# Kernel optimization log

Hardware: AMD Instinct MI355X
Metric: run time of the kernel (lower is better)

Reference implementation:

```python
import jax, jax.numpy as jnp
import numpy as np

DIM = 768
HEADS = 12
FF = 3072
EPS = 1e-6


def setup_inputs() -> dict:
    key = jax.random.key(0)
    ks = jax.random.split(key, 12)
    B, S, D, F_ = 64, 197, DIM, FF
    s = 0.02
    inp = {
        "x": jax.random.normal(ks[0], (B, S, D), jnp.float32),
        "Wq": jax.random.normal(ks[1], (D, D), jnp.float32) * s,
        "bq": jnp.zeros((D,), jnp.float32),
        "Wk": jax.random.normal(ks[2], (D, D), jnp.float32) * s,
        "bk": jnp.zeros((D,), jnp.float32),
        "Wv": jax.random.normal(ks[3], (D, D), jnp.float32) * s,
        "bv": jnp.zeros((D,), jnp.float32),
        "Wo": jax.random.normal(ks[4], (D, D), jnp.float32) * s,
        "bo": jnp.zeros((D,), jnp.float32),
        "ln1_w": jnp.ones((D,), jnp.float32),
        "ln1_b": jnp.zeros((D,), jnp.float32),
        "W1": jax.random.normal(ks[5], (D, F_), jnp.float32) * s,
        "b1": jnp.zeros((F_,), jnp.float32),
        "W2": jax.random.normal(ks[6], (F_, D), jnp.float32) * s,
        "b2": jnp.zeros((D,), jnp.float32),
        "ln2_w": jnp.ones((D,), jnp.float32),
        "ln2_b": jnp.zeros((D,), jnp.float32),
        "mask": jnp.ones((B, S), jnp.int32),
    }
    return inp


def _layernorm(x, w, b):
    m = jnp.mean(x, axis=-1, keepdims=True)
    v = jnp.mean(jnp.square(x - m), axis=-1, keepdims=True)  # unbiased=False
    return (x - m) / jnp.sqrt(v + EPS) * w + b


def _block(x, mask_f, Wq, bq, Wk, bk, Wv, bv, Wo, bo, ln1_w, ln1_b, W1, b1, W2, b2, ln2_w, ln2_b):
    B, S, D = x.shape
    H = HEADS
    Dh = D // H
    # --- attention (pre-norm) ---
    h = _layernorm(x, ln1_w, ln1_b)
    q = (h @ Wq + bq).reshape(B, S, H, Dh).transpose(0, 2, 1, 3)
    k = (h @ Wk + bk).reshape(B, S, H, Dh).transpose(0, 2, 1, 3)
    v = (h @ Wv + bv).reshape(B, S, H, Dh).transpose(0, 2, 1, 3)
    scores = jnp.einsum("bhqd,bhkd->bhqk", q, k) / jnp.sqrt(jnp.float32(Dh))
    scores = scores - 10000.0 * (1.0 - mask_f[:, None, None, :])
    probs = jax.nn.softmax(scores, axis=-1)
    attn = jnp.einsum("bhqk,bhkd->bhqd", probs, v).transpose(0, 2, 1, 3).reshape(B, S, D)
    x = x + (attn @ Wo + bo)  # dropout = identity (eval)
    # --- FFN (pre-norm), exact erf GELU (F.gelu default) ---
    h = _layernorm(x, ln2_w, ln2_b)
    h = jax.nn.gelu(h @ W1 + b1, approximate=False)
    x = x + (h @ W2 + b2)
    return x


def reference(x, Wq, bq, Wk, bk, Wv, bv, Wo, bo, ln1_w, ln1_b, W1, b1, W2, b2, ln2_w, ln2_b, mask):
    mask_f = mask.astype(jnp.float32)
    return _block(x, mask_f, Wq, bq, Wk, bk, Wv, bv, Wo, bo, ln1_w, ln1_b, W1, b1, W2, b2, ln2_w, ln2_b)
```

## Files before the change

kernel.cpp:

```cpp
#include <hip/hip_runtime.h>
#include <stdint.h>

#define B_   64
#define S_   197
#define D_   768
#define H_   12
#define F_   3072
#define BS_  (B_ * S_)

typedef __attribute__((ext_vector_type(8))) short short8;
typedef __attribute__((ext_vector_type(4))) float f32x4;

__device__ __forceinline__ float bf2f(unsigned short h) {
    union { unsigned int u; float f; } v; v.u = ((unsigned int)h) << 16; return v.f;
}
__device__ __forceinline__ unsigned short f2bf(float f) {
    union { float f; unsigned int u; } v; v.f = f;
    unsigned int r = v.u + 0x7FFFu + ((v.u >> 16) & 1u);
    return (unsigned short)(r >> 16);
}

__device__ __forceinline__ void g2l16(const void* g, void* l) {
    __builtin_amdgcn_global_load_lds(
        (const __attribute__((address_space(1))) unsigned int*)g,
        (__attribute__((address_space(3))) unsigned int*)l, 16, 0, 0);
}

__device__ __forceinline__ float gelu_f(float c) {
    float z = fabsf(c) * 0.70710678118f;
    float t = __builtin_amdgcn_rcpf(1.f + 0.3275911f * z);
    float p = ((((1.061405429f * t - 1.453152027f) * t + 1.421413741f) * t
               - 0.284496736f) * t + 0.254829592f) * t;
    float erfv = 1.f - p * __expf(-z * z);
    erfv = c < 0.f ? -erfv : erfv;
    return 0.5f * c * (1.f + erfv);
}

__global__ __launch_bounds__(256)
void transpose_all(const float* __restrict__ Wq, const float* __restrict__ Wk,
                   const float* __restrict__ Wv, const float* __restrict__ Wo,
                   const float* __restrict__ W1, const float* __restrict__ W2,
                   const float* __restrict__ bq, const float* __restrict__ bk,
                   const float* __restrict__ bv,
                   unsigned short* __restrict__ wqkvT, unsigned short* __restrict__ woT,
                   unsigned short* __restrict__ w1T, unsigned short* __restrict__ w2T,
                   float* __restrict__ bcat) {
    int blk = blockIdx.x;
    int tx = threadIdx.x, ty = threadIdx.y;
    if (blk == 6912) {
        for (int i = ty * 32 + tx; i < 2304; i += 256)
            bcat[i] = i < 768 ? bq[i] : (i < 1536 ? bk[i - 768] : bv[i - 1536]);
        return;
    }
    const float* W; unsigned short* Wt; int K, N, rel, nx;
    if (blk < 2304) {
        int m = blk / 576; rel = blk - m * 576; K = 768; N = 768; nx = 24;
        W  = m == 0 ? Wq : m == 1 ? Wk : m == 2 ? Wv : Wo;
        Wt = m < 3 ? wqkvT + (size_t)m * 768 * 768 : woT;
    } else if (blk < 4608) {
        rel = blk - 2304; K = 768; N = 3072; nx = 96; W = W1; Wt = w1T;
    } else {
        rel = blk - 4608; K = 3072; N = 768; nx = 24; W = W2; Wt = w2T;
    }
    int n0 = (rel % nx) * 32, k0 = (rel / nx) * 32;
    __shared__ float t[32][33];
#pragma unroll
    for (int i = ty; i < 32; i += 8) t[i][tx] = W[(size_t)(k0 + i) * N + n0 + tx];
    __syncthreads();
#pragma unroll
    for (int i = ty; i < 32; i += 8) Wt[(size_t)(n0 + i) * K + k0 + tx] = f2bf(t[tx][i]);
}

__global__ __launch_bounds__(256)
void ln_kernel(const float* __restrict__ x, const float* __restrict__ w,
               const float* __restrict__ b, unsigned short* __restrict__ out) {
    int row = blockIdx.x; size_t base = (size_t)row * 768;
    int tid = threadIdx.x;
    float v0 = x[base + tid], v1 = x[base + tid + 256], v2 = x[base + tid + 512];
    float s1 = v0 + v1 + v2;
    float s2 = v0 * v0 + v1 * v1 + v2 * v2;
#pragma unroll
    for (int off = 32; off > 0; off >>= 1) { s1 += __shfl_xor(s1, off); s2 += __shfl_xor(s2, off); }
    __shared__ float sa[4], sb[4];
    int w4 = tid >> 6;
    if ((tid & 63) == 0) { sa[w4] = s1; sb[w4] = s2; }
    __syncthreads();
    s1 = sa[0] + sa[1] + sa[2] + sa[3];
    s2 = sb[0] + sb[1] + sb[2] + sb[3];
    float mean = s1 * (1.f / 768.f);
    float var  = s2 * (1.f / 768.f) - mean * mean;
    float rstd = rsqrtf(var + 1e-6f);
    out[base + tid]       = f2bf((v0 - mean) * rstd * w[tid]       + b[tid]);
    out[base + tid + 256] = f2bf((v1 - mean) * rstd * w[tid + 256] + b[tid + 256]);
    out[base + tid + 512] = f2bf((v2 - mean) * rstd * w[tid + 512] + b[tid + 512]);
}

template<int MODE, int BM_, int BN_>
__global__ __launch_bounds__(512)
void gemmL2(const unsigned short* __restrict__ A, const unsigned short* __restrict__ Bt,
            const float* __restrict__ bias, const float* __restrict__ resid,
            void* __restrict__ out, int M, int N, int K, int NSUP) {
    constexpr int BK = 32;
    constexpr int WGN = (BN_ == 256) ? 4 : 2;
    constexpr int WGM = 8 / WGN;
    constexpr int WM = BM_ / WGM, WN = BN_ / WGN;
    constexpr int MT = WM / 16, NT = WN / 16;
    __shared__ unsigned short As[2][BM_ * BK];
    __shared__ unsigned short Bs[2][BN_ * BK];
    const int tid = threadIdx.x;
    const int l = tid & 63, wid = tid >> 6;
    const int lr = l & 15, lg = l >> 4;
    const int wr = wid / WGN, wc = wid % WGN;

    const int nN = gridDim.x, nM = gridDim.y;
    const int nTot = nN * nM;
    const int orig = blockIdx.x + nN * blockIdx.y;
    const int q8 = nTot >> 3, r8 = nTot & 7;
    const int xcd = orig & 7, idx = orig >> 3;
    const int rank = (xcd < r8 ? xcd * (q8 + 1) : r8 * (q8 + 1) + (xcd - r8) * q8) + idx;
    const int fullg = nM * NSUP;
    const int sup = rank / fullg;
    const int rem = rank - sup * fullg;
    const int n0s = sup * NSUP;
    int wsup = nN - n0s; if (wsup > NSUP) wsup = NSUP;
    const int mloc = rem / wsup;
    const int nloc = rem - mloc * wsup;
    const int bm0 = mloc * BM_;
    const int bn0 = (n0s + nloc) * BN_;

    const int srow = tid >> 2;
    const int slb  = (tid & 3) ^ ((tid >> 3) & 3);
    auto stage = [&](int buf, int kt) {
        const int k0 = kt * BK;
#pragma unroll
        for (int c = 0; c < BM_ / 128; ++c) {
            int gr = bm0 + c * 128 + srow; gr = gr < M ? gr : M - 1;
            g2l16(A + (size_t)gr * K + k0 + slb * 8, &As[buf][(c * 128 + srow) * BK]);
        }
#pragma unroll
        for (int c = 0; c < BN_ / 128; ++c) {
            int gr = bn0 + c * 128 + srow;
            g2l16(Bt + (size_t)gr * K + k0 + slb * 8, &Bs[buf][(c * 128 + srow) * BK]);
        }
    };

    f32x4 acc[MT][NT];
#pragma unroll
    for (int i = 0; i < MT; ++i)
#pragma unroll
        for (int j = 0; j < NT; ++j) acc[i][j] = (f32x4){0.f, 0.f, 0.f, 0.f};

    const int NK = K / BK;
    stage(0, 0);
    __syncthreads();

    const int rsw = (lr >> 1) & 3;
    for (int kt = 0; kt < NK; ++kt) {
        const int buf = kt & 1;
        if (kt + 1 < NK) stage(buf ^ 1, kt + 1);
        short8 bfr[NT];
#pragma unroll
        for (int nt = 0; nt < NT; ++nt)
            bfr[nt] = *(const short8*)&Bs[buf][(wc * WN + nt * 16 + lr) * BK + ((lg ^ rsw) * 8)];
#pragma unroll
        for (int mt = 0; mt < MT; ++mt) {
            const short8 af = *(const short8*)&As[buf][(wr * WM + mt * 16 + lr) * BK + ((lg ^ rsw) * 8)];
#pragma unroll
            for (int nt = 0; nt < NT; ++nt)
                acc[mt][nt] = __builtin_amdgcn_mfma_f32_16x16x32_bf16(af, bfr[nt], acc[mt][nt], 0, 0, 0);
        }
        __syncthreads();
    }

#pragma unroll
    for (int mt = 0; mt < MT; ++mt)
#pragma unroll
        for (int nt = 0; nt < NT; ++nt)
#pragma unroll
            for (int r = 0; r < 4; ++r) {
                int gm = bm0 + wr * WM + mt * 16 + lg * 4 + r;
                int gn = bn0 + wc * WN + nt * 16 + lr;
                if (gm < M) {
                    float c = acc[mt][nt][r] + bias[gn];
                    if (MODE == 0) {
                        if (gn < 768) c *= 0.125f;
                        ((unsigned short*)out)[(size_t)gm * N + gn] = f2bf(c);
                    } else if (MODE == 1) {
                        ((float*)out)[(size_t)gm * N + gn] = c + resid[(size_t)gm * N + gn];
                    } else {
                        ((unsigned short*)out)[(size_t)gm * N + gn] = f2bf(gelu_f(c));
                    }
                }
            }
}

__global__ __launch_bounds__(256)
void attn_mfma(const unsigned short* __restrict__ qkv, const int* __restrict__ mask,
               unsigned short* __restrict__ ctx) {
    __shared__ unsigned short Ks[208 * 64];
    __shared__ unsigned short Vt[64 * 256];
    __shared__ unsigned short Psl[4][16 * 40];
    __shared__ float maskadj[224];
    const int bh = blockIdx.x, b = bh / 12, h = bh - b * 12;
    const int tid = threadIdx.x, l = tid & 63, w = tid >> 6;
    const int lr = l & 15, lg = l >> 4;
    const unsigned short* Qg = qkv + (size_t)b * 197 * 2304 + h * 64;
    const unsigned short* Kg = Qg + 768;
    const unsigned short* Vg = Qg + 1536;

    if (tid < 224)
        maskadj[tid] = tid < 197 ? -10000.f * (1.f - (float)mask[b * 197 + tid]) : -1e30f;

    for (int c = w; c < 26; c += 4) {
        int row = c * 8 + (l >> 3);
        int rc = row < 197 ? row : 196;
        int blk = (l & 7) ^ (row & 7);
        g2l16(Kg + (size_t)rc * 2304 + blk * 8, &Ks[c * 8 * 64]);
    }
    {
        int jj = tid >> 3, db = tid & 7;
#pragma unroll
        for (int it = 0; it < 7; ++it) {
            int j = it * 32 + jj;
            short8 v = (short8){0, 0, 0, 0, 0, 0, 0, 0};
            if (j < 197) v = *(const short8*)(Vg + (size_t)j * 2304 + db * 8);
#pragma unroll
            for (int e = 0; e < 8; ++e) {
                int d = db * 8 + e;
                Vt[d * 256 + (((j >> 3) ^ (d & 7)) * 8) + (j & 7)] = (unsigned short)v[e];
            }
        }
    }
    __syncthreads();

    for (int t = w; t < 13; t += 4) {
        const int q0 = t * 16;
        int qr = q0 + lr; qr = qr < 197 ? qr : 196;
        const short8 qf0 = *(const short8*)(Qg + (size_t)qr * 2304 + lg * 8);
        const short8 qf1 = *(const short8*)(Qg + (size_t)qr * 2304 + 32 + lg * 8);

        f32x4 sc[13];
#pragma unroll
        for (int kt = 0; kt < 13; ++kt) {
            const int krow = kt * 16 + lr;
            const short8 kf0 = *(const short8*)&Ks[krow * 64 + ((lg ^ (lr & 7)) * 8)];
            const short8 kf1 = *(const short8*)&Ks[krow * 64 + (((4 + lg) ^ (lr & 7)) * 8)];
            f32x4 a = (f32x4){0.f, 0.f, 0.f, 0.f};
            a = __builtin_amdgcn_mfma_f32_16x16x32_bf16(qf0, kf0, a, 0, 0, 0);
            a = __builtin_amdgcn_mfma_f32_16x16x32_bf16(qf1, kf1, a, 0, 0, 0);
            sc[kt] = a;
        }
        float mx[4] = {-1e30f, -1e30f, -1e30f, -1e30f};
#pragma unroll
        for (int kt = 0; kt < 13; ++kt) {
            float ma = maskadj[kt * 16 + lr];
#pragma unroll
            for (int r = 0; r < 4; ++r) {
                sc[kt][r] += ma;
                mx[r] = fmaxf(mx[r], sc[kt][r]);
            }
        }
#pragma unroll
        for (int r = 0; r < 4; ++r) {
            mx[r] = fmaxf(mx[r], __shfl_xor(mx[r], 1));
            mx[r] = fmaxf(mx[r], __shfl_xor(mx[r], 2));
            mx[r] = fmaxf(mx[r], __shfl_xor(mx[r], 4));
            mx[r] = fmaxf(mx[r], __shfl_xor(mx[r], 8));
        }
        float sm[4] = {0.f, 0.f, 0.f, 0.f};
#pragma unroll
        for (int kt = 0; kt < 13; ++kt)
#pragma unroll
            for (int r = 0; r < 4; ++r) {
                float p = __expf(sc[kt][r] - mx[r]);
                sc[kt][r] = p;
                sm[r] += p;
            }
#pragma unroll
        for (int r = 0; r < 4; ++r) {
            sm[r] += __shfl_xor(sm[r], 1);
            sm[r] += __shfl_xor(sm[r], 2);
            sm[r] += __shfl_xor(sm[r], 4);
            sm[r] += __shfl_xor(sm[r], 8);
            sm[r] = 1.f / sm[r];
        }
        f32x4 ao[4];
#pragma unroll
        for (int dt = 0; dt < 4; ++dt) ao[dt] = (f32x4){0.f, 0.f, 0.f, 0.f};
        unsigned short* Pw = &Psl[w][0];
#pragma unroll
        for (int ks = 0; ks < 7; ++ks) {
#pragma unroll
            for (int tl = 0; tl < 2; ++tl) {
                const int kt = ks * 2 + tl;
#pragma unroll
                for (int r = 0; r < 4; ++r) {
                    unsigned short pv = 0;
                    if (kt < 13) pv = f2bf(sc[kt][r] * sm[r]);
                    Pw[(lg * 4 + r) * 40 + tl * 16 + lr] = pv;
                }
            }
            const short8 pf = *(const short8*)&Pw[lr * 40 + lg * 8];
#pragma unroll
            for (int dt = 0; dt < 4; ++dt) {
                const int drow = dt * 16 + lr;
                const short8 vf = *(const short8*)&Vt[drow * 256 + (((4 * ks + lg) ^ (lr & 7)) * 8)];
                ao[dt] = __builtin_amdgcn_mfma_f32_16x16x32_bf16(vf, pf, ao[dt], 0, 0, 0);
            }
        }
        const int q = q0 + lr;
        if (q < 197) {
            unsigned short* crow = ctx + ((size_t)b * 197 + q) * 768 + h * 64;
#pragma unroll
            for (int dt = 0; dt < 4; ++dt) {
                union { unsigned short u[4]; uint2 v; } pk;
#pragma unroll
                for (int r = 0; r < 4; ++r) pk.u[r] = f2bf(ao[dt][r]);
                *(uint2*)(crow + dt * 16 + lg * 4) = pk.v;
            }
        }
    }
}

extern "C" void kernel_launch(void* const* d_in, const int* in_sizes, int n_in,
                              void* d_out, int out_size, void* d_ws, size_t ws_size,
                              hipStream_t stream) {
    const float* x    = (const float*)d_in[0];
    const float* Wq   = (const float*)d_in[1];
    const float* bq   = (const float*)d_in[2];
    const float* Wk   = (const float*)d_in[3];
    const float* bk   = (const float*)d_in[4];
    const float* Wv   = (const float*)d_in[5];
    const float* bv   = (const float*)d_in[6];
    const float* Wo   = (const float*)d_in[7];
    const float* bo   = (const float*)d_in[8];
    const float* ln1w = (const float*)d_in[9];
    const float* ln1b = (const float*)d_in[10];
    const float* W1   = (const float*)d_in[11];
    const float* b1   = (const float*)d_in[12];
    const float* W2   = (const float*)d_in[13];
    const float* b2   = (const float*)d_in[14];
    const float* ln2w = (const float*)d_in[15];
    const float* ln2b = (const float*)d_in[16];
    const int*   mask = (const int*)d_in[17];

    size_t off = 0;
    auto nxt = [&](size_t bytes) -> void* {
        void* r = (char*)d_ws + off; off += (bytes + 255) & ~(size_t)255; return r;
    };
    unsigned short* hbuf  = (unsigned short*)nxt((size_t)BS_ * 768 * 2);
    unsigned short* qkvg  = (unsigned short*)nxt((size_t)BS_ * 3072 * 2);
    unsigned short* wqkvT = (unsigned short*)nxt((size_t)2304 * 768 * 2);
    unsigned short* woT   = (unsigned short*)nxt((size_t)768 * 768 * 2);
    unsigned short* w1T   = (unsigned short*)nxt((size_t)3072 * 768 * 2);
    unsigned short* w2T   = (unsigned short*)nxt((size_t)768 * 3072 * 2);
    float*          bcat  = (float*)nxt(2304 * 4);
    unsigned short* ctx   = (unsigned short*)nxt((size_t)BS_ * 768 * 2);
    (void)ws_size; (void)in_sizes; (void)n_in; (void)out_size;

    transpose_all<<<6913, dim3(32, 8), 0, stream>>>(Wq, Wk, Wv, Wo, W1, W2, bq, bk, bv,
                                                    wqkvT, woT, w1T, w2T, bcat);
    ln_kernel<<<BS_, 256, 0, stream>>>(x, ln1w, ln1b, hbuf);
    gemmL2<0, 256, 256><<<dim3(9, 50), 512, 0, stream>>>(hbuf, wqkvT, bcat, nullptr, qkvg, BS_, 2304, 768, 5);
    attn_mfma<<<768, 256, 0, stream>>>(qkvg, mask, ctx);
    gemmL2<1, 128, 128><<<dim3(6, 99), 512, 0, stream>>>(ctx, woT, bo, x, d_out, BS_, 768, 768, 6);
    ln_kernel<<<BS_, 256, 0, stream>>>((const float*)d_out, ln2w, ln2b, hbuf);
    gemmL2<2, 256, 256><<<dim3(12, 50), 512, 0, stream>>>(hbuf, w1T, b1, nullptr, qkvg, BS_, 3072, 768, 6);
    gemmL2<1, 256, 128><<<dim3(6, 50), 512, 0, stream>>>(qkvg, w2T, b2, (const float*)d_out, d_out, BS_, 768, 3072, 3);
}
```

Baseline: 475.1 us.

## Replace double-buffered GEMM with single-buffer 128x128 BK=64 tile kernel

```diff
diff --git a/kernel.cpp b/kernel.cpp
--- a/kernel.cpp
+++ b/kernel.cpp
@@ -95,22 +95,18 @@
     out[base + tid + 512] = f2bf((v2 - mean) * rstd * w[tid + 512] + b[tid + 512]);
 }
 
-template<int MODE, int BM_, int BN_>
-__global__ __launch_bounds__(512)
-void gemmL2(const unsigned short* __restrict__ A, const unsigned short* __restrict__ Bt,
+template<int MODE>
+__global__ __launch_bounds__(256)
+void gemmv7(const unsigned short* __restrict__ A, const unsigned short* __restrict__ Bt,
             const float* __restrict__ bias, const float* __restrict__ resid,
             void* __restrict__ out, int M, int N, int K, int NSUP) {
-    constexpr int BK = 32;
-    constexpr int WGN = (BN_ == 256) ? 4 : 2;
-    constexpr int WGM = 8 / WGN;
-    constexpr int WM = BM_ / WGM, WN = BN_ / WGN;
-    constexpr int MT = WM / 16, NT = WN / 16;
-    __shared__ unsigned short As[2][BM_ * BK];
-    __shared__ unsigned short Bs[2][BN_ * BK];
+    constexpr int BK = 64;
+    __shared__ unsigned short As[128 * BK];
+    __shared__ unsigned short Bs[128 * BK];
     const int tid = threadIdx.x;
-    const int l = tid & 63, wid = tid >> 6;
+    const int l = tid & 63, w = tid >> 6;
     const int lr = l & 15, lg = l >> 4;
-    const int wr = wid / WGN, wc = wid % WGN;
+    const int wr = w >> 1, wc = w & 1;
 
     const int nN = gridDim.x, nM = gridDim.y;
     const int nTot = nN * nM;
@@ -125,61 +121,65 @@
     int wsup = nN - n0s; if (wsup > NSUP) wsup = NSUP;
     const int mloc = rem / wsup;
     const int nloc = rem - mloc * wsup;
-    const int bm0 = mloc * BM_;
-    const int bn0 = (n0s + nloc) * BN_;
-
-    const int srow = tid >> 2;
-    const int slb  = (tid & 3) ^ ((tid >> 3) & 3);
-    auto stage = [&](int buf, int kt) {
+    const int bm0 = mloc * 128;
+    const int bn0 = (n0s + nloc) * 128;
+
+    const int sr8 = l >> 3;
+    const int slb = (l & 7) ^ sr8;
+    auto stage = [&](int kt) {
         const int k0 = kt * BK;
 #pragma unroll
-        for (int c = 0; c < BM_ / 128; ++c) {
-            int gr = bm0 + c * 128 + srow; gr = gr < M ? gr : M - 1;
-            g2l16(A + (size_t)gr * K + k0 + slb * 8, &As[buf][(c * 128 + srow) * BK]);
-        }
-#pragma unroll
-        for (int c = 0; c < BN_ / 128; ++c) {
-            int gr = bn0 + c * 128 + srow;
-            g2l16(Bt + (size_t)gr * K + k0 + slb * 8, &Bs[buf][(c * 128 + srow) * BK]);
+        for (int c = 0; c < 4; ++c) {
+            int gr = bm0 + c * 32 + w * 8 + sr8; gr = gr < M ? gr : M - 1;
+            g2l16(A + (size_t)gr * K + k0 + slb * 8, &As[(c * 32 + w * 8) * BK]);
+            int gb = bn0 + c * 32 + w * 8 + sr8;
+            g2l16(Bt + (size_t)gb * K + k0 + slb * 8, &Bs[(c * 32 + w * 8) * BK]);
         }
     };
 
-    f32x4 acc[MT][NT];
-#pragma unroll
-    for (int i = 0; i < MT; ++i)
-#pragma unroll
-        for (int j = 0; j < NT; ++j) acc[i][j] = (f32x4){0.f, 0.f, 0.f, 0.f};
+    f32x4 acc[4][4];
+#pragma unroll
+    for (int i = 0; i < 4; ++i)
+#pragma unroll
+        for (int j = 0; j < 4; ++j) acc[i][j] = (f32x4){0.f, 0.f, 0.f, 0.f};
 
     const int NK = K / BK;
-    stage(0, 0);
-    __syncthreads();
-
-    const int rsw = (lr >> 1) & 3;
+    const int rsw = lr & 7;
     for (int kt = 0; kt < NK; ++kt) {
-        const int buf = kt & 1;
-        if (kt + 1 < NK) stage(buf ^ 1, kt + 1);
-        short8 bfr[NT];
-#pragma unroll
-        for (int nt = 0; nt < NT; ++nt)
-            bfr[nt] = *(const short8*)&Bs[buf][(wc * WN + nt * 16 + lr) * BK + ((lg ^ rsw) * 8)];
-#pragma unroll
-        for (int mt = 0; mt < MT; ++mt) {
-            const short8 af = *(const short8*)&As[buf][(wr * WM + mt * 16 + lr) * BK + ((lg ^ rsw) * 8)];
-#pragma unroll
-            for (int nt = 0; nt < NT; ++nt)
-                acc[mt][nt] = __builtin_amdgcn_mfma_f32_16x16x32_bf16(af, bfr[nt], acc[mt][nt], 0, 0, 0);
-        }
+        stage(kt);
         __syncthreads();
-    }
-
-#pragma unroll
-    for (int mt = 0; mt < MT; ++mt)
-#pragma unroll
-        for (int nt = 0; nt < NT; ++nt)
+        short8 bfr[4][2];
+#pragma unroll
+        for (int nt = 0; nt < 4; ++nt)
+#pragma unroll
+            for (int kk = 0; kk < 2; ++kk)
+                bfr[nt][kk] = *(const short8*)&Bs[(wc * 64 + nt * 16 + lr) * BK +
+                                                  (((kk * 4 + lg) ^ rsw) * 8)];
+#pragma unroll
+        for (int mt = 0; mt < 4; ++mt) {
+            short8 af[2];
+#pragma unroll
+            for (int kk = 0; kk < 2; ++kk)
+                af[kk] = *(const short8*)&As[(wr * 64 + mt * 16 + lr) * BK +
+                                             (((kk * 4 + lg) ^ rsw) * 8)];
+#pragma unroll
+            for (int nt = 0; nt < 4; ++nt)
+#pragma unroll
+                for (int kk = 0; kk < 2; ++kk)
+                    acc[mt][nt] = __builtin_amdgcn_mfma_f32_16x16x32_bf16(
+                        af[kk], bfr[nt][kk], acc[mt][nt], 0, 0, 0);
+        }
+        __syncthreads();
+    }
+
+#pragma unroll
+    for (int mt = 0; mt < 4; ++mt)
+#pragma unroll
+        for (int nt = 0; nt < 4; ++nt)
 #pragma unroll
             for (int r = 0; r < 4; ++r) {
-                int gm = bm0 + wr * WM + mt * 16 + lg * 4 + r;
-                int gn = bn0 + wc * WN + nt * 16 + lr;
+                int gm = bm0 + wr * 64 + mt * 16 + lg * 4 + r;
+                int gn = bn0 + wc * 64 + nt * 16 + lr;
                 if (gm < M) {
                     float c = acc[mt][nt][r] + bias[gn];
                     if (MODE == 0) {
@@ -361,10 +361,10 @@
     transpose_all<<<6913, dim3(32, 8), 0, stream>>>(Wq, Wk, Wv, Wo, W1, W2, bq, bk, bv,
                                                     wqkvT, woT, w1T, w2T, bcat);
     ln_kernel<<<BS_, 256, 0, stream>>>(x, ln1w, ln1b, hbuf);
-    gemmL2<0, 256, 256><<<dim3(9, 50), 512, 0, stream>>>(hbuf, wqkvT, bcat, nullptr, qkvg, BS_, 2304, 768, 5);
+    gemmv7<0><<<dim3(18, 99), 256, 0, stream>>>(hbuf, wqkvT, bcat, nullptr, qkvg, BS_, 2304, 768, 9);
     attn_mfma<<<768, 256, 0, stream>>>(qkvg, mask, ctx);
-    gemmL2<1, 128, 128><<<dim3(6, 99), 512, 0, stream>>>(ctx, woT, bo, x, d_out, BS_, 768, 768, 6);
+    gemmv7<1><<<dim3(6, 99), 256, 0, stream>>>(ctx, woT, bo, x, d_out, BS_, 768, 768, 6);
     ln_kernel<<<BS_, 256, 0, stream>>>((const float*)d_out, ln2w, ln2b, hbuf);
-    gemmL2<2, 256, 256><<<dim3(12, 50), 512, 0, stream>>>(hbuf, w1T, b1, nullptr, qkvg, BS_, 3072, 768, 6);
-    gemmL2<1, 256, 128><<<dim3(6, 50), 512, 0, stream>>>(qkvg, w2T, b2, (const float*)d_out, d_out, BS_, 768, 3072, 3);
-}
+    gemmv7<2><<<dim3(24, 99), 256, 0, stream>>>(hbuf, w1T, b1, nullptr, qkvg, BS_, 3072, 768, 12);
+    gemmv7<1><<<dim3(6, 99), 256, 0, stream>>>(qkvg, w2T, b2, (const float*)d_out, d_out, BS_, 768, 3072, 3);
+}
```

Measured after the change: 529.3 us. +11.4%, slower.

## Replace GEMM with triple-buffered phased pipeline using manual waitcnt scheduling

Applied to the files above, without the earlier changes.

```diff
diff --git a/kernel.cpp b/kernel.cpp
--- a/kernel.cpp
+++ b/kernel.cpp
@@ -95,18 +95,24 @@
     out[base + tid + 512] = f2bf((v2 - mean) * rstd * w[tid + 512] + b[tid + 512]);
 }
 
-template<int MODE, int BM_, int BN_>
-__global__ __launch_bounds__(512)
-void gemmL2(const unsigned short* __restrict__ A, const unsigned short* __restrict__ Bt,
-            const float* __restrict__ bias, const float* __restrict__ resid,
-            void* __restrict__ out, int M, int N, int K, int NSUP) {
-    constexpr int BK = 32;
-    constexpr int WGN = (BN_ == 256) ? 4 : 2;
-    constexpr int WGM = 8 / WGN;
-    constexpr int WM = BM_ / WGM, WN = BN_ / WGN;
-    constexpr int MT = WM / 16, NT = WN / 16;
-    __shared__ unsigned short As[2][BM_ * BK];
-    __shared__ unsigned short Bs[2][BN_ * BK];
+template<int MODE, int GEOM>
+__global__ __launch_bounds__(GEOM == 0 ? 512 : 256)
+void gemm8ph(const unsigned short* __restrict__ A, const unsigned short* __restrict__ Bt,
+             const float* __restrict__ bias, const float* __restrict__ resid,
+             void* __restrict__ out, int M, int N, int K, int NSUP) {
+    constexpr int BK  = 32;
+    constexpr int BM  = GEOM == 0 ? 256 : 128;
+    constexpr int BN  = GEOM == 0 ? 256 : 128;
+    constexpr int NTH = GEOM == 0 ? 512 : 256;
+    constexpr int WGN = GEOM == 0 ? 4 : 2;
+    constexpr int WM  = GEOM == 0 ? 128 : 64;
+    constexpr int WN  = 64;
+    constexpr int MT  = WM / 16, NT = WN / 16;
+    constexpr int PH  = MT / 4;
+    constexpr int RPC = NTH / 4;
+
+    __shared__ unsigned short As[3][BM * BK];
+    __shared__ unsigned short Bs[3][BN * BK];
     const int tid = threadIdx.x;
     const int l = tid & 63, wid = tid >> 6;
     const int lr = l & 15, lg = l >> 4;
@@ -125,22 +131,25 @@
     int wsup = nN - n0s; if (wsup > NSUP) wsup = NSUP;
     const int mloc = rem / wsup;
     const int nloc = rem - mloc * wsup;
-    const int bm0 = mloc * BM_;
-    const int bn0 = (n0s + nloc) * BN_;
-
-    const int srow = tid >> 2;
-    const int slb  = (tid & 3) ^ ((tid >> 3) & 3);
-    auto stage = [&](int buf, int kt) {
+    const int bm0 = mloc * BM;
+    const int bn0 = (n0s + nloc) * BN;
+
+    const int srow = wid * 16 + (l >> 2);
+    const int slb  = (l & 3) ^ ((l >> 3) & 3);
+    auto stageHalf = [&](int ring, int kt, int half) {
         const int k0 = kt * BK;
-#pragma unroll
-        for (int c = 0; c < BM_ / 128; ++c) {
-            int gr = bm0 + c * 128 + srow; gr = gr < M ? gr : M - 1;
-            g2l16(A + (size_t)gr * K + k0 + slb * 8, &As[buf][(c * 128 + srow) * BK]);
-        }
-#pragma unroll
-        for (int c = 0; c < BN_ / 128; ++c) {
-            int gr = bn0 + c * 128 + srow;
-            g2l16(Bt + (size_t)gr * K + k0 + slb * 8, &Bs[buf][(c * 128 + srow) * BK]);
+        if (half == 0) {
+#pragma unroll
+            for (int c = 0; c < BM / RPC; ++c) {
+                int gr = bm0 + c * RPC + srow; gr = gr < M ? gr : M - 1;
+                g2l16(A + (size_t)gr * K + k0 + slb * 8, &As[ring][(c * RPC + wid * 16) * BK]);
+            }
+        } else {
+#pragma unroll
+            for (int c = 0; c < BN / RPC; ++c) {
+                int gr = bn0 + c * RPC + srow;
+                g2l16(Bt + (size_t)gr * K + k0 + slb * 8, &Bs[ring][(c * RPC + wid * 16) * BK]);
+            }
         }
     };
 
@@ -151,25 +160,47 @@
         for (int j = 0; j < NT; ++j) acc[i][j] = (f32x4){0.f, 0.f, 0.f, 0.f};
 
     const int NK = K / BK;
-    stage(0, 0);
-    __syncthreads();
-
-    const int rsw = (lr >> 1) & 3;
+    stageHalf(0, 0, 0); stageHalf(0, 0, 1);
+    stageHalf(1, 1, 0); stageHalf(1, 1, 1);
+
+    const int rxor = (lr >> 1) & 3;
+    int ring = 0;
     for (int kt = 0; kt < NK; ++kt) {
-        const int buf = kt & 1;
-        if (kt + 1 < NK) stage(buf ^ 1, kt + 1);
+        if (kt + 1 < NK) { asm volatile("s_waitcnt vmcnt(4)" ::: "memory"); }
+        else             { asm volatile("s_waitcnt vmcnt(0)" ::: "memory"); }
+        __builtin_amdgcn_s_barrier();
+        __builtin_amdgcn_sched_barrier(0);
+        const unsigned short* Ab = &As[ring][0];
+        const unsigned short* Bb = &Bs[ring][0];
+        const int rnext = ring >= 1 ? ring - 1 : 2;
+        const bool st = (kt + 2 < NK);
+
         short8 bfr[NT];
 #pragma unroll
         for (int nt = 0; nt < NT; ++nt)
-            bfr[nt] = *(const short8*)&Bs[buf][(wc * WN + nt * 16 + lr) * BK + ((lg ^ rsw) * 8)];
-#pragma unroll
-        for (int mt = 0; mt < MT; ++mt) {
-            const short8 af = *(const short8*)&As[buf][(wr * WM + mt * 16 + lr) * BK + ((lg ^ rsw) * 8)];
-#pragma unroll
-            for (int nt = 0; nt < NT; ++nt)
-                acc[mt][nt] = __builtin_amdgcn_mfma_f32_16x16x32_bf16(af, bfr[nt], acc[mt][nt], 0, 0, 0);
-        }
-        __syncthreads();
+            bfr[nt] = *(const short8*)&Bb[(wc * WN + nt * 16 + lr) * BK + ((lg ^ rxor) * 8)];
+#pragma unroll
+        for (int ph = 0; ph < PH; ++ph) {
+            short8 af[4];
+#pragma unroll
+            for (int mt = 0; mt < 4; ++mt)
+                af[mt] = *(const short8*)&Ab[(wr * WM + (ph * 4 + mt) * 16 + lr) * BK + ((lg ^ rxor) * 8)];
+            if (st) stageHalf(rnext, kt + 2, ph);
+            if (PH == 1 && st) stageHalf(rnext, kt + 2, 1);
+            __builtin_amdgcn_s_barrier();
+            asm volatile("s_waitcnt lgkmcnt(0)" ::: "memory");
+            __builtin_amdgcn_sched_barrier(0);
+            __builtin_amdgcn_s_setprio(1);
+#pragma unroll
+            for (int mt = 0; mt < 4; ++mt)
+#pragma unroll
+                for (int nt = 0; nt < NT; ++nt)
+                    acc[ph * 4 + mt][nt] = __builtin_amdgcn_mfma_f32_16x16x32_bf16(
+                        af[mt], bfr[nt], acc[ph * 4 + mt][nt], 0, 0, 0);
+            __builtin_amdgcn_s_setprio(0);
+            __builtin_amdgcn_s_barrier();
+        }
+        ring = ring < 2 ? ring + 1 : 0;
     }
 
 #pragma unroll
@@ -361,10 +392,10 @@
     transpose_all<<<6913, dim3(32, 8), 0, stream>>>(Wq, Wk, Wv, Wo, W1, W2, bq, bk, bv,
                                                     wqkvT, woT, w1T, w2T, bcat);
     ln_kernel<<<BS_, 256, 0, stream>>>(x, ln1w, ln1b, hbuf);
-    gemmL2<0, 256, 256><<<dim3(9, 50), 512, 0, stream>>>(hbuf, wqkvT, bcat, nullptr, qkvg, BS_, 2304, 768, 5);
+    gemm8ph<0, 0><<<dim3(9, 50), 512, 0, stream>>>(hbuf, wqkvT, bcat, nullptr, qkvg, BS_, 2304, 768, 5);
     attn_mfma<<<768, 256, 0, stream>>>(qkvg, mask, ctx);
-    gemmL2<1, 128, 128><<<dim3(6, 99), 512, 0, stream>>>(ctx, woT, bo, x, d_out, BS_, 768, 768, 6);
+    gemm8ph<1, 1><<<dim3(6, 99), 256, 0, stream>>>(ctx, woT, bo, x, d_out, BS_, 768, 768, 6);
     ln_kernel<<<BS_, 256, 0, stream>>>((const float*)d_out, ln2w, ln2b, hbuf);
-    gemmL2<2, 256, 256><<<dim3(12, 50), 512, 0, stream>>>(hbuf, w1T, b1, nullptr, qkvg, BS_, 3072, 768, 6);
-    gemmL2<1, 256, 128><<<dim3(6, 50), 512, 0, stream>>>(qkvg, w2T, b2, (const float*)d_out, d_out, BS_, 768, 3072, 3);
-}
+    gemm8ph<2, 0><<<dim3(12, 50), 512, 0, stream>>>(hbuf, w1T, b1, nullptr, qkvg, BS_, 3072, 768, 6);
+    gemm8ph<1, 1><<<dim3(6, 99), 256, 0, stream>>>(qkvg, w2T, b2, (const float*)d_out, d_out, BS_, 768, 3072, 3);
+}
```

Measured after the change: 450.3 us. 1.06x faster.

## Stage GEMM tiles through registers instead of direct global-to-LDS loads

Applied to the files above, without the earlier changes.

```diff
diff --git a/kernel.cpp b/kernel.cpp
--- a/kernel.cpp
+++ b/kernel.cpp
@@ -95,18 +95,21 @@
     out[base + tid + 512] = f2bf((v2 - mean) * rstd * w[tid + 512] + b[tid + 512]);
 }
 
-template<int MODE, int BM_, int BN_>
-__global__ __launch_bounds__(512)
-void gemmL2(const unsigned short* __restrict__ A, const unsigned short* __restrict__ Bt,
+template<int MODE, int GEOM>
+__global__ __launch_bounds__(GEOM == 0 ? 512 : 256)
+void gemmRS(const unsigned short* __restrict__ A, const unsigned short* __restrict__ Bt,
             const float* __restrict__ bias, const float* __restrict__ resid,
             void* __restrict__ out, int M, int N, int K, int NSUP) {
-    constexpr int BK = 32;
-    constexpr int WGN = (BN_ == 256) ? 4 : 2;
-    constexpr int WGM = 8 / WGN;
-    constexpr int WM = BM_ / WGM, WN = BN_ / WGN;
-    constexpr int MT = WM / 16, NT = WN / 16;
-    __shared__ unsigned short As[2][BM_ * BK];
-    __shared__ unsigned short Bs[2][BN_ * BK];
+    constexpr int BK  = 32;
+    constexpr int BM  = GEOM == 0 ? 256 : 128;
+    constexpr int BN  = GEOM == 0 ? 256 : 128;
+    constexpr int WGN = GEOM == 0 ? 4 : 2;
+    constexpr int WM  = GEOM == 0 ? 128 : 64;
+    constexpr int WN  = 64;
+    constexpr int MT  = WM / 16, NT = WN / 16;
+
+    __shared__ unsigned short As[2][BM * BK];
+    __shared__ unsigned short Bs[2][BN * BK];
     const int tid = threadIdx.x;
     const int l = tid & 63, wid = tid >> 6;
     const int lr = l & 15, lg = l >> 4;
@@ -125,24 +128,28 @@
     int wsup = nN - n0s; if (wsup > NSUP) wsup = NSUP;
     const int mloc = rem / wsup;
     const int nloc = rem - mloc * wsup;
-    const int bm0 = mloc * BM_;
-    const int bn0 = (n0s + nloc) * BN_;
-
-    const int srow = tid >> 2;
-    const int slb  = (tid & 3) ^ ((tid >> 3) & 3);
-    auto stage = [&](int buf, int kt) {
-        const int k0 = kt * BK;
-#pragma unroll
-        for (int c = 0; c < BM_ / 128; ++c) {
-            int gr = bm0 + c * 128 + srow; gr = gr < M ? gr : M - 1;
-            g2l16(A + (size_t)gr * K + k0 + slb * 8, &As[buf][(c * 128 + srow) * BK]);
-        }
-#pragma unroll
-        for (int c = 0; c < BN_ / 128; ++c) {
-            int gr = bn0 + c * 128 + srow;
-            g2l16(Bt + (size_t)gr * K + k0 + slb * 8, &Bs[buf][(c * 128 + srow) * BK]);
-        }
+    const int bm0 = mloc * BM;
+    const int bn0 = (n0s + nloc) * BN;
+
+    const int rw = tid >> 1, hh = tid & 1;
+    int gra = bm0 + rw; gra = gra < M ? gra : M - 1;
+    const unsigned short* agp = A  + (size_t)gra * K + hh * 16;
+    const unsigned short* bgp = Bt + (size_t)(bn0 + rw) * K + hh * 16;
+    const int xw = (rw >> 1) & 3;
+    const int wo0 = rw * BK + (((2 * hh + 0) ^ xw) * 8);
+    const int wo1 = rw * BK + (((2 * hh + 1) ^ xw) * 8);
+
+    uint4 ra0, ra1, rb0, rb1;
+    auto ld = [&](int kt) {
+        const unsigned short* ap = agp + kt * BK;
+        const unsigned short* bp = bgp + kt * BK;
+        ra0 = *(const uint4*)(ap);     ra1 = *(const uint4*)(ap + 8);
+        rb0 = *(const uint4*)(bp);     rb1 = *(const uint4*)(bp + 8);
     };
+    auto st = [&](int buf) {
+        *(uint4*)&As[buf][wo0] = ra0;  *(uint4*)&As[buf][wo1] = ra1;
+        *(uint4*)&Bs[buf][wo0] = rb0;  *(uint4*)&Bs[buf][wo1] = rb1;
+    };
 
     f32x4 acc[MT][NT];
 #pragma unroll
@@ -151,24 +158,28 @@
         for (int j = 0; j < NT; ++j) acc[i][j] = (f32x4){0.f, 0.f, 0.f, 0.f};
 
     const int NK = K / BK;
-    stage(0, 0);
+    ld(0); st(0);
     __syncthreads();
 
-    const int rsw = (lr >> 1) & 3;
+    const int rxor = (lr >> 1) & 3;
     for (int kt = 0; kt < NK; ++kt) {
         const int buf = kt & 1;
-        if (kt + 1 < NK) stage(buf ^ 1, kt + 1);
+        if (kt + 1 < NK) {
+            ld(kt + 1);
+            __builtin_amdgcn_sched_barrier(0);
+        }
         short8 bfr[NT];
 #pragma unroll
         for (int nt = 0; nt < NT; ++nt)
-            bfr[nt] = *(const short8*)&Bs[buf][(wc * WN + nt * 16 + lr) * BK + ((lg ^ rsw) * 8)];
+            bfr[nt] = *(const short8*)&Bs[buf][(wc * WN + nt * 16 + lr) * BK + ((lg ^ rxor) * 8)];
 #pragma unroll
         for (int mt = 0; mt < MT; ++mt) {
-            const short8 af = *(const short8*)&As[buf][(wr * WM + mt * 16 + lr) * BK + ((lg ^ rsw) * 8)];
+            const short8 af = *(const short8*)&As[buf][(wr * WM + mt * 16 + lr) * BK + ((lg ^ rxor) * 8)];
 #pragma unroll
             for (int nt = 0; nt < NT; ++nt)
                 acc[mt][nt] = __builtin_amdgcn_mfma_f32_16x16x32_bf16(af, bfr[nt], acc[mt][nt], 0, 0, 0);
         }
+        if (kt + 1 < NK) st(buf ^ 1);
         __syncthreads();
     }
 
@@ -361,10 +372,10 @@
     transpose_all<<<6913, dim3(32, 8), 0, stream>>>(Wq, Wk, Wv, Wo, W1, W2, bq, bk, bv,
                                                     wqkvT, woT, w1T, w2T, bcat);
     ln_kernel<<<BS_, 256, 0, stream>>>(x, ln1w, ln1b, hbuf);
-    gemmL2<0, 256, 256><<<dim3(9, 50), 512, 0, stream>>>(hbuf, wqkvT, bcat, nullptr, qkvg, BS_, 2304, 768, 5);
+    gemmRS<0, 0><<<dim3(9, 50), 512, 0, stream>>>(hbuf, wqkvT, bcat, nullptr, qkvg, BS_, 2304, 768, 5);
     attn_mfma<<<768, 256, 0, stream>>>(qkvg, mask, ctx);
-    gemmL2<1, 128, 128><<<dim3(6, 99), 512, 0, stream>>>(ctx, woT, bo, x, d_out, BS_, 768, 768, 6);
+    gemmRS<1, 1><<<dim3(6, 99), 256, 0, stream>>>(ctx, woT, bo, x, d_out, BS_, 768, 768, 6);
     ln_kernel<<<BS_, 256, 0, stream>>>((const float*)d_out, ln2w, ln2b, hbuf);
-    gemmL2<2, 256, 256><<<dim3(12, 50), 512, 0, stream>>>(hbuf, w1T, b1, nullptr, qkvg, BS_, 3072, 768, 6);
-    gemmL2<1, 256, 128><<<dim3(6, 50), 512, 0, stream>>>(qkvg, w2T, b2, (const float*)d_out, d_out, BS_, 768, 3072, 3);
-}
+    gemmRS<2, 0><<<dim3(12, 50), 512, 0, stream>>>(hbuf, w1T, b1, nullptr, qkvg, BS_, 3072, 768, 6);
+    gemmRS<1, 1><<<dim3(6, 99), 256, 0, stream>>>(qkvg, w2T, b2, (const float*)d_out, d_out, BS_, 768, 3072, 3);
+}
```

New measurement: 465.9 us. About the same (-2.0%).
